# Kernel optimization log

Hardware: AMD Instinct MI355X
Metric: run time of the kernel (lower is better)

## Reference

```python
import jax, jax.numpy as jnp
import numpy as np

N_NODES = 50000
N_EDGES = 800000
N_GRAPHS = 8
D_IN, D_HID, D_OUT = 128, 128, 64


def setup_inputs() -> dict:
    key = jax.random.key(0)
    ks = jax.random.split(key, 8)
    x = jax.random.normal(ks[0], (N_NODES, D_IN), jnp.float32)
    src = jax.random.randint(ks[1], (N_EDGES,), 0, N_NODES, dtype=jnp.int32)
    dst = jax.random.randint(ks[2], (N_EDGES,), 0, N_NODES, dtype=jnp.int32)
    graph_id = jnp.sort(jax.random.randint(ks[3], (N_NODES,), 0, N_GRAPHS, dtype=jnp.int32))
    s1 = 1.0 / np.sqrt(D_IN)
    s2 = 1.0 / np.sqrt(D_HID)
    W1 = jax.random.normal(ks[4], (D_IN, D_HID), jnp.float32) * s1
    b1 = jnp.zeros((D_HID,), jnp.float32)
    W2 = jax.random.normal(ks[5], (D_HID, D_HID), jnp.float32) * s2
    b2 = jnp.zeros((D_HID,), jnp.float32)
    Wl = jax.random.normal(ks[6], (D_HID, D_OUT), jnp.float32) * s2
    bl = jnp.zeros((D_OUT,), jnp.float32)
    return dict(x=x, W1=W1, b1=b1, W2=W2, b2=b2, Wl=Wl, bl=bl,
                src=src, dst=dst, graph_id=graph_id)


def _graph_conv(x, W, b, src, dst):
    # DGL GraphConv, norm='both': h' = D_in^{-1/2} A (D_out^{-1/2} x W) + b
    n = x.shape[0]
    ones = jnp.ones((src.shape[0],), x.dtype)
    out_deg = jax.ops.segment_sum(ones, src, num_segments=n)
    in_deg = jax.ops.segment_sum(ones, dst, num_segments=n)
    norm_src = jax.lax.rsqrt(jnp.clip(out_deg, 1.0))  # [N]
    norm_dst = jax.lax.rsqrt(jnp.clip(in_deg, 1.0))   # [N]
    h = (x * norm_src[:, None]) @ W                    # [N, D]
    agg = jax.ops.segment_sum(h[src], dst, num_segments=n)  # gather-scatter SpMM
    return agg * norm_dst[:, None] + b


def reference(x, W1, b1, W2, b2, Wl, bl, src, dst, graph_id):
    h = jax.nn.relu(_graph_conv(x, W1, b1, src, dst))
    h = _graph_conv(h, W2, b2, src, dst)
    # dgl.mean_nodes over batched graph: per-graph mean of node features
    cnt = jax.ops.segment_sum(jnp.ones((x.shape[0],), x.dtype), graph_id,
                              num_segments=N_GRAPHS)
    pooled = jax.ops.segment_sum(h, graph_id, num_segments=N_GRAPHS)
    means = pooled / jnp.clip(cnt, 1.0)[:, None]       # [B, D_HID]
    return means @ Wl + bl                              # [B, D_OUT]
```

## Files before the change

kernel.cpp:

```cpp
#include <hip/hip_runtime.h>
#include <hip/hip_bf16.h>

#define N_NODES 50000
#define N_EDGES 800000
#define N_GRAPHS 8
#define MAXDEG 64
#define NRANGE 4
#define NCHUNK 64
#define RSZ (N_NODES / NRANGE)
#define CHE (N_EDGES / NCHUNK)

typedef __attribute__((ext_vector_type(8))) short short8;
typedef __attribute__((ext_vector_type(4))) float floatx4;
typedef __attribute__((ext_vector_type(2))) float floatx2;

static __device__ __forceinline__ ushort f2b(float f) {
    union { float f; unsigned u; } v; v.f = f;
    return (ushort)((v.u + 0x7FFF + ((v.u >> 16) & 1)) >> 16);
}
static __device__ __forceinline__ float b2f(unsigned u) {
    union { unsigned u; float f; } v; v.u = u << 16;
    return v.f;
}
static __device__ __forceinline__ unsigned char f2q(float f) {
    int p = __builtin_amdgcn_cvt_pk_fp8_f32(f, f, 0, false);
    return (unsigned char)(p & 0xff);
}

__global__ __launch_bounds__(1024) void prep_kernel(
    const int* __restrict__ src, const int* __restrict__ dst,
    const float* __restrict__ W1, const float* __restrict__ W2,
    const int* __restrict__ gid,
    ushort* __restrict__ counts_in, ushort* __restrict__ counts_out,
    ushort* __restrict__ Wt1, ushort* __restrict__ Wt2,
    int* __restrict__ start)
{
    int b = blockIdx.x, t = threadIdx.x;
    if (b < 256) {
        __shared__ unsigned h[RSZ];
        int c = b & (NCHUNK - 1), r = b >> 6;
        int lo = r * RSZ;
        for (int j = t; j < RSZ; j += 1024) h[j] = 0;
        __syncthreads();
        int ebeg = c * CHE, eend = ebeg + CHE;
        for (int i = ebeg + t; i < eend; i += 1024) {
            int s = src[i], d = dst[i];
            unsigned ds = (unsigned)(d - lo);
            if (ds < RSZ) atomicAdd(&h[ds >> 1], 1u << ((ds & 1) * 16));
            unsigned ss = (unsigned)(s - lo);
            if (ss < RSZ) atomicAdd(&h[(RSZ / 2) + (ss >> 1)], 1u << ((ss & 1) * 16));
        }
        __syncthreads();
        unsigned* ci = (unsigned*)(counts_in  + (size_t)c * N_NODES + lo);
        unsigned* co = (unsigned*)(counts_out + (size_t)c * N_NODES + lo);
        for (int j = t; j < RSZ / 2; j += 1024) {
            ci[j] = h[j];
            co[j] = h[(RSZ / 2) + j];
        }
    } else if (b < 272) {
        int i = (b - 256) * 1024 + t;
        int c = i >> 7, k = i & 127;
        Wt1[i] = f2b(W1[k * 128 + c]);
        Wt2[i] = f2b(W2[k * 128 + c]);
    } else {
        int i = (b - 272) * 1024 + t;
        if (i < N_NODES) {
            int g = gid[i];
            int gp = (i == 0) ? -1 : gid[i - 1];
            for (int k = gp + 1; k <= g; ++k) start[k] = i;
            if (i == N_NODES - 1)
                for (int k = g + 1; k <= N_GRAPHS; ++k) start[k] = N_NODES;
        }
    }
}

__global__ __launch_bounds__(256) void scan_kernel(
    const ushort* __restrict__ counts_in, const ushort* __restrict__ counts_out,
    ushort* __restrict__ base, int* __restrict__ in_deg,
    float* __restrict__ ns, float* __restrict__ nd)
{
    int v = blockIdx.x * 256 + threadIdx.x;
    if (v >= N_NODES) return;
    unsigned od = 0;
    #pragma unroll 8
    for (int c = 0; c < NCHUNK; ++c) od += counts_out[(size_t)c * N_NODES + v];
    unsigned run = 0;
    #pragma unroll 8
    for (int c = 0; c < NCHUNK; ++c) {
        base[(size_t)c * N_NODES + v] = (ushort)run;
        run += counts_in[(size_t)c * N_NODES + v];
    }
    in_deg[v] = (int)run;
    ns[v] = rsqrtf(fmaxf((float)od, 1.f));
    nd[v] = rsqrtf(fmaxf((float)run, 1.f));
}

__global__ __launch_bounds__(1024) void scatter_kernel(
    const int* __restrict__ src, const int* __restrict__ dst,
    const ushort* __restrict__ base, ushort* __restrict__ slot)
{
    __shared__ unsigned h[RSZ / 2];
    int t = threadIdx.x;
    int c = blockIdx.x & (NCHUNK - 1), r = blockIdx.x >> 6;
    int lo = r * RSZ;
    const unsigned* bp = (const unsigned*)(base + (size_t)c * N_NODES + lo);
    for (int j = t; j < RSZ / 2; j += 1024) h[j] = bp[j];
    __syncthreads();
    int ebeg = c * CHE, eend = ebeg + CHE;
    for (int i = ebeg + t; i < eend; i += 1024) {
        int d = dst[i];
        unsigned ds = (unsigned)(d - lo);
        if (ds < RSZ) {
            int sh = (ds & 1) * 16;
            unsigned old = atomicAdd(&h[ds >> 1], 1u << sh);
            unsigned pos = (old >> sh) & 0xffff;
            if (pos < MAXDEG) slot[(size_t)d * MAXDEG + pos] = (ushort)src[i];
        }
    }
}

template<int FP32_IN>
__global__ __launch_bounds__(256, 2) void mfma_gemm_kernel(
    const void* __restrict__ Xv, const float* __restrict__ scale,
    const ushort* __restrict__ Wt, unsigned char* __restrict__ Y, int n)
{
    int t = threadIdx.x;
    int wv = t >> 6, lane = t & 63;
    int m = lane & 15, q = lane >> 4;
    short8 B[8][4];
    #pragma unroll
    for (int cb = 0; cb < 8; ++cb)
        #pragma unroll
        for (int kb = 0; kb < 4; ++kb)
            B[cb][kb] = *(const short8*)&Wt[(size_t)(cb * 16 + m) * 128 + kb * 32 + q * 8];

    int ntile = n >> 4;
    int gw = blockIdx.x * 4 + wv;
    for (int tile = gw; tile < ntile; tile += 2048) {
        int row = tile * 16 + m;
        short8 a[4];
        if (FP32_IN) {
            const float* X = (const float*)Xv;
            float s = scale[row];
            #pragma unroll
            for (int kb = 0; kb < 4; ++kb) {
                const float* p = X + (size_t)row * 128 + kb * 32 + q * 8;
                float4 f0 = *(const float4*)p;
                float4 f1 = *(const float4*)(p + 4);
                short8 av;
                av[0] = (short)f2b(f0.x * s); av[1] = (short)f2b(f0.y * s);
                av[2] = (short)f2b(f0.z * s); av[3] = (short)f2b(f0.w * s);
                av[4] = (short)f2b(f1.x * s); av[5] = (short)f2b(f1.y * s);
                av[6] = (short)f2b(f1.z * s); av[7] = (short)f2b(f1.w * s);
                a[kb] = av;
            }
        } else {
            const ushort* X = (const ushort*)Xv;
            #pragma unroll
            for (int kb = 0; kb < 4; ++kb)
                a[kb] = *(const short8*)(X + (size_t)row * 128 + kb * 32 + q * 8);
        }
        floatx4 acc[8] = {};
        #pragma unroll
        for (int cb = 0; cb < 8; ++cb)
            #pragma unroll
            for (int kb = 0; kb < 4; ++kb)
                acc[cb] = __builtin_amdgcn_mfma_f32_16x16x32_bf16(a[kb], B[cb][kb], acc[cb], 0, 0, 0);
        int rowbase = tile * 16 + q * 4;
        #pragma unroll
        for (int cb = 0; cb < 8; ++cb)
            #pragma unroll
            for (int r = 0; r < 4; ++r)
                Y[(size_t)(rowbase + r) * 128 + cb * 16 + m] = f2q(acc[cb][r]);
    }
}

__global__ __launch_bounds__(256) void spmm_fp8_kernel(
    const unsigned char* __restrict__ H, const int* __restrict__ in_deg,
    const ushort* __restrict__ slot, const float* __restrict__ norm_dst,
    const float* __restrict__ norm_src, const float* __restrict__ bias,
    ushort* __restrict__ Y, int relu_scale)
{
    int wid = (blockIdx.x * blockDim.x + threadIdx.x) >> 6;
    if (wid >= N_NODES / 8) return;
    int lane = threadIdx.x & 63;
    int g = lane >> 3;
    int j = lane & 7;
    int node = wid * 8 + g;
    int cnt = min(in_deg[node], MAXDEG);
    float ndv = norm_dst[node];
    const ushort* lst = slot + (size_t)node * MAXDEG;

    int cm = cnt;
    cm = max(cm, __shfl_xor(cm, 8, 64));
    cm = max(cm, __shfl_xor(cm, 16, 64));
    cm = max(cm, __shfl_xor(cm, 32, 64));

    float acc[16] = {};
    for (int e0 = 0; e0 < cm; e0 += 8) {
        int sl = lst[e0 + j];
        #pragma unroll
        for (int k = 0; k < 8; ++k) {
            if (e0 + k < cnt) {
                int s = __shfl(sl, g * 8 + k, 64);
                uint4 v = *(const uint4*)&H[(size_t)s * 128 + j * 16];
                floatx2 p;
                p = __builtin_amdgcn_cvt_pk_f32_fp8((int)v.x, false); acc[0] += p.x;  acc[1] += p.y;
                p = __builtin_amdgcn_cvt_pk_f32_fp8((int)v.x, true);  acc[2] += p.x;  acc[3] += p.y;
                p = __builtin_amdgcn_cvt_pk_f32_fp8((int)v.y, false); acc[4] += p.x;  acc[5] += p.y;
                p = __builtin_amdgcn_cvt_pk_f32_fp8((int)v.y, true);  acc[6] += p.x;  acc[7] += p.y;
                p = __builtin_amdgcn_cvt_pk_f32_fp8((int)v.z, false); acc[8] += p.x;  acc[9] += p.y;
                p = __builtin_amdgcn_cvt_pk_f32_fp8((int)v.z, true);  acc[10] += p.x; acc[11] += p.y;
                p = __builtin_amdgcn_cvt_pk_f32_fp8((int)v.w, false); acc[12] += p.x; acc[13] += p.y;
                p = __builtin_amdgcn_cvt_pk_f32_fp8((int)v.w, true);  acc[14] += p.x; acc[15] += p.y;
            }
        }
    }

    int c16 = j * 16;
    float r[16];
    #pragma unroll
    for (int u = 0; u < 4; ++u) {
        float4 bv = *(const float4*)&bias[c16 + u * 4];
        r[u * 4 + 0] = acc[u * 4 + 0] * ndv + bv.x;
        r[u * 4 + 1] = acc[u * 4 + 1] * ndv + bv.y;
        r[u * 4 + 2] = acc[u * 4 + 2] * ndv + bv.z;
        r[u * 4 + 3] = acc[u * 4 + 3] * ndv + bv.w;
    }
    if (relu_scale) {
        float nsv = norm_src[node];
        #pragma unroll
        for (int u = 0; u < 16; ++u) r[u] = fmaxf(r[u], 0.f) * nsv;
    }
    uint4 o0, o1;
    o0.x = (unsigned)f2b(r[0])  | ((unsigned)f2b(r[1])  << 16);
    o0.y = (unsigned)f2b(r[2])  | ((unsigned)f2b(r[3])  << 16);
    o0.z = (unsigned)f2b(r[4])  | ((unsigned)f2b(r[5])  << 16);
    o0.w = (unsigned)f2b(r[6])  | ((unsigned)f2b(r[7])  << 16);
    o1.x = (unsigned)f2b(r[8])  | ((unsigned)f2b(r[9])  << 16);
    o1.y = (unsigned)f2b(r[10]) | ((unsigned)f2b(r[11]) << 16);
    o1.z = (unsigned)f2b(r[12]) | ((unsigned)f2b(r[13]) << 16);
    o1.w = (unsigned)f2b(r[14]) | ((unsigned)f2b(r[15]) << 16);
    uint4* yp = (uint4*)&Y[(size_t)node * 128 + c16];
    yp[0] = o0;
    yp[1] = o1;
}

__global__ __launch_bounds__(256) void pool_kernel(
    const ushort* __restrict__ H, const int* __restrict__ start,
    float* __restrict__ part)
{
    __shared__ float red[128];
    int t = threadIdx.x;
    int g = blockIdx.x >> 5, j = blockIdx.x & 31;
    int beg0 = start[g], len = start[g + 1] - beg0;
    int sbeg = beg0 + (int)(((long long)len * j) >> 5);
    int send = beg0 + (int)(((long long)len * (j + 1)) >> 5);
    int wv = t >> 6, lane = t & 63;
    int rg = lane >> 4;
    int c8 = (lane & 15) * 8;
    float acc[8] = {};
    for (int v = sbeg + wv * 4 + rg; v < send; v += 16) {
        uint4 u = *(const uint4*)&H[(size_t)v * 128 + c8];
        acc[0] += b2f(u.x & 0xffff); acc[1] += b2f(u.x >> 16);
        acc[2] += b2f(u.y & 0xffff); acc[3] += b2f(u.y >> 16);
        acc[4] += b2f(u.z & 0xffff); acc[5] += b2f(u.z >> 16);
        acc[6] += b2f(u.w & 0xffff); acc[7] += b2f(u.w >> 16);
    }
    #pragma unroll
    for (int k = 0; k < 8; ++k) {
        acc[k] += __shfl_xor(acc[k], 16, 64);
        acc[k] += __shfl_xor(acc[k], 32, 64);
    }
    if (t < 128) red[t] = 0.f;
    __syncthreads();
    if (lane < 16) {
        #pragma unroll
        for (int k = 0; k < 8; ++k) atomicAdd(&red[c8 + k], acc[k]);
    }
    __syncthreads();
    if (t < 128) part[(size_t)blockIdx.x * 128 + t] = red[t];
}

__global__ __launch_bounds__(512) void head_kernel(
    const float* __restrict__ part, const int* __restrict__ start,
    const float* __restrict__ Wl, const float* __restrict__ bl,
    float* __restrict__ out)
{
    __shared__ float means[N_GRAPHS * 128];
    int t = threadIdx.x;
    for (int i = t; i < N_GRAPHS * 128; i += 512) {
        int g = i >> 7, k = i & 127;
        float s = 0.f;
        #pragma unroll 8
        for (int j = 0; j < 32; ++j) s += part[(size_t)(g * 32 + j) * 128 + k];
        float cnt = (float)(start[g + 1] - start[g]);
        means[i] = s / fmaxf(cnt, 1.f);
    }
    __syncthreads();
    int g = t >> 6, c = t & 63;
    float acc = bl[c];
    #pragma unroll 8
    for (int k = 0; k < 128; ++k)
        acc = fmaf(means[g * 128 + k], Wl[k * 64 + c], acc);
    out[g * 64 + c] = acc;
}

extern "C" void kernel_launch(void* const* d_in, const int* in_sizes, int n_in,
                              void* d_out, int out_size, void* d_ws, size_t ws_size,
                              hipStream_t stream) {
    const float* x   = (const float*)d_in[0];
    const float* W1  = (const float*)d_in[1];
    const float* b1  = (const float*)d_in[2];
    const float* W2  = (const float*)d_in[3];
    const float* b2  = (const float*)d_in[4];
    const float* Wl  = (const float*)d_in[5];
    const float* bl  = (const float*)d_in[6];
    const int*   src = (const int*)d_in[7];
    const int*   dst = (const int*)d_in[8];
    const int*   gid = (const int*)d_in[9];

    const int n = N_NODES;

    char* ws = (char*)d_ws;
    size_t off = 0;
    auto alloc = [&](size_t bytes) { size_t o = off; off += (bytes + 255) & ~(size_t)255; return o; };
    unsigned char* hA = (unsigned char*)(ws + alloc((size_t)n * 128));
    ushort* hB        = (ushort*)(ws + alloc((size_t)n * 128 * 2));
    ushort* slot      = (ushort*)(ws + alloc((size_t)n * MAXDEG * 2));
    ushort* counts_in = (ushort*)(ws + alloc((size_t)NCHUNK * n * 2));
    ushort* counts_out= (ushort*)(ws + alloc((size_t)NCHUNK * n * 2));
    ushort* basev     = (ushort*)(ws + alloc((size_t)NCHUNK * n * 2));
    float* norm_src   = (float*) (ws + alloc((size_t)n * 4));
    float* norm_dst   = (float*) (ws + alloc((size_t)n * 4));
    int*   in_deg     = (int*)   (ws + alloc((size_t)n * 4));
    int*   startb     = (int*)   (ws + alloc((size_t)(N_GRAPHS + 1) * 4));
    ushort* Wt1       = (ushort*)(ws + alloc((size_t)128 * 128 * 2));
    ushort* Wt2       = (ushort*)(ws + alloc((size_t)128 * 128 * 2));
    float* part       = (float*) (ws + alloc((size_t)N_GRAPHS * 32 * 128 * 4));

    int spmm_blocks = (N_NODES / 8 + 3) / 4;

    prep_kernel<<<321, 1024, 0, stream>>>(src, dst, W1, W2, gid,
                                          counts_in, counts_out, Wt1, Wt2, startb);
    scan_kernel<<<(n + 255) / 256, 256, 0, stream>>>(counts_in, counts_out, basev,
                                                     in_deg, norm_src, norm_dst);
    scatter_kernel<<<NRANGE * NCHUNK, 1024, 0, stream>>>(src, dst, basev, slot);
    mfma_gemm_kernel<1><<<512, 256, 0, stream>>>(x, norm_src, Wt1, hA, n);
    spmm_fp8_kernel<<<spmm_blocks, 256, 0, stream>>>(hA, in_deg, slot, norm_dst,
                                                     norm_src, b1, hB, 1);
    mfma_gemm_kernel<0><<<512, 256, 0, stream>>>(hB, nullptr, Wt2, hA, n);
    spmm_fp8_kernel<<<spmm_blocks, 256, 0, stream>>>(hA, in_deg, slot, norm_dst,
                                                     nullptr, b2, hB, 0);
    pool_kernel<<<N_GRAPHS * 32, 256, 0, stream>>>(hB, startb, part);
    head_kernel<<<1, 512, 0, stream>>>(part, startb, Wl, bl, (float*)d_out);
}
```

Baseline: 199.7 us.

## Sort destination nodes by in-degree to balance SpMM wavefront work

Builds a degree histogram during the scan and adds a kernel that produces a permutation of nodes grouped by in-degree. Each SpMM wavefront then processes 8 nodes with similar degree, so the inner loop bound (the max degree among the 8) no longer wastes iterations on divergent lanes. The cost is one extra kernel launch, an indirect perm load, and scattered output rows, which lose the write locality of contiguous node order.

```diff
diff --git a/kernel.cpp b/kernel.cpp
--- a/kernel.cpp
+++ b/kernel.cpp
@@ -33,7 +33,7 @@
     const int* __restrict__ gid,
     ushort* __restrict__ counts_in, ushort* __restrict__ counts_out,
     ushort* __restrict__ Wt1, ushort* __restrict__ Wt2,
-    int* __restrict__ start)
+    int* __restrict__ start, unsigned* __restrict__ binz)
 {
     int b = blockIdx.x, t = threadIdx.x;
     if (b < 256) {
@@ -71,28 +71,61 @@
             if (i == N_NODES - 1)
                 for (int k = g + 1; k <= N_GRAPHS; ++k) start[k] = N_NODES;
         }
+        if (b == 320 && t >= 848 && t < 978) binz[t - 848] = 0;
     }
 }
 
 __global__ __launch_bounds__(256) void scan_kernel(
     const ushort* __restrict__ counts_in, const ushort* __restrict__ counts_out,
     ushort* __restrict__ base, int* __restrict__ in_deg,
-    float* __restrict__ ns, float* __restrict__ nd)
-{
-    int v = blockIdx.x * 256 + threadIdx.x;
-    if (v >= N_NODES) return;
-    unsigned od = 0;
-    #pragma unroll 8
-    for (int c = 0; c < NCHUNK; ++c) od += counts_out[(size_t)c * N_NODES + v];
-    unsigned run = 0;
-    #pragma unroll 8
-    for (int c = 0; c < NCHUNK; ++c) {
-        base[(size_t)c * N_NODES + v] = (ushort)run;
-        run += counts_in[(size_t)c * N_NODES + v];
-    }
-    in_deg[v] = (int)run;
-    ns[v] = rsqrtf(fmaxf((float)od, 1.f));
-    nd[v] = rsqrtf(fmaxf((float)run, 1.f));
+    float* __restrict__ ns, float* __restrict__ nd, unsigned* __restrict__ bins)
+{
+    __shared__ unsigned hist[MAXDEG + 1];
+    int t = threadIdx.x;
+    if (t < MAXDEG + 1) hist[t] = 0;
+    __syncthreads();
+    int v = blockIdx.x * 256 + t;
+    if (v < N_NODES) {
+        unsigned od = 0;
+        #pragma unroll 8
+        for (int c = 0; c < NCHUNK; ++c) od += counts_out[(size_t)c * N_NODES + v];
+        unsigned run = 0;
+        #pragma unroll 8
+        for (int c = 0; c < NCHUNK; ++c) {
+            base[(size_t)c * N_NODES + v] = (ushort)run;
+            run += counts_in[(size_t)c * N_NODES + v];
+        }
+        in_deg[v] = (int)run;
+        ns[v] = rsqrtf(fmaxf((float)od, 1.f));
+        nd[v] = rsqrtf(fmaxf((float)run, 1.f));
+        atomicAdd(&hist[min((int)run, MAXDEG)], 1u);
+    }
+    __syncthreads();
+    if (t < MAXDEG + 1 && hist[t]) atomicAdd(&bins[t], hist[t]);
+}
+
+__global__ __launch_bounds__(256) void perm_kernel(
+    const int* __restrict__ in_deg, const unsigned* __restrict__ bins,
+    unsigned* __restrict__ bincur, int* __restrict__ perm)
+{
+    __shared__ unsigned bh[MAXDEG + 1], bstart[MAXDEG + 1], sbin[MAXDEG + 1];
+    int t = threadIdx.x;
+    if (t < MAXDEG + 1) { bh[t] = 0; sbin[t] = bins[t]; }
+    __syncthreads();
+    int v = blockIdx.x * 256 + t;
+    int cb = 0; unsigned rank = 0;
+    if (v < N_NODES) {
+        cb = min(in_deg[v], MAXDEG);
+        rank = atomicAdd(&bh[cb], 1u);
+    }
+    __syncthreads();
+    if (t < MAXDEG + 1) {
+        unsigned b0 = 0;
+        for (int k = 0; k < t; ++k) b0 += sbin[k];
+        bstart[t] = b0 + atomicAdd(&bincur[t], bh[t]);
+    }
+    __syncthreads();
+    if (v < N_NODES) perm[bstart[cb] + rank] = v;
 }
 
 __global__ __launch_bounds__(1024) void scatter_kernel(
@@ -179,14 +212,14 @@
     const unsigned char* __restrict__ H, const int* __restrict__ in_deg,
     const ushort* __restrict__ slot, const float* __restrict__ norm_dst,
     const float* __restrict__ norm_src, const float* __restrict__ bias,
-    ushort* __restrict__ Y, int relu_scale)
+    const int* __restrict__ perm, ushort* __restrict__ Y, int relu_scale)
 {
     int wid = (blockIdx.x * blockDim.x + threadIdx.x) >> 6;
     if (wid >= N_NODES / 8) return;
     int lane = threadIdx.x & 63;
     int g = lane >> 3;
     int j = lane & 7;
-    int node = wid * 8 + g;
+    int node = perm[wid * 8 + g];
     int cnt = min(in_deg[node], MAXDEG);
     float ndv = norm_dst[node];
     const ushort* lst = slot + (size_t)node * MAXDEG;
@@ -338,20 +371,27 @@
     ushort* Wt1       = (ushort*)(ws + alloc((size_t)128 * 128 * 2));
     ushort* Wt2       = (ushort*)(ws + alloc((size_t)128 * 128 * 2));
     float* part       = (float*) (ws + alloc((size_t)N_GRAPHS * 32 * 128 * 4));
+    unsigned* binz    = (unsigned*)(ws + alloc((size_t)130 * 4));
+    int*   permv      = (int*)   (ws + alloc((size_t)n * 4));
+
+    unsigned* bins   = binz;
+    unsigned* bincur = binz + 65;
 
     int spmm_blocks = (N_NODES / 8 + 3) / 4;
+    int node_blocks = (n + 255) / 256;
 
     prep_kernel<<<321, 1024, 0, stream>>>(src, dst, W1, W2, gid,
-                                          counts_in, counts_out, Wt1, Wt2, startb);
-    scan_kernel<<<(n + 255) / 256, 256, 0, stream>>>(counts_in, counts_out, basev,
-                                                     in_deg, norm_src, norm_dst);
+                                          counts_in, counts_out, Wt1, Wt2, startb, binz);
+    scan_kernel<<<node_blocks, 256, 0, stream>>>(counts_in, counts_out, basev,
+                                                 in_deg, norm_src, norm_dst, bins);
+    perm_kernel<<<node_blocks, 256, 0, stream>>>(in_deg, bins, bincur, permv);
     scatter_kernel<<<NRANGE * NCHUNK, 1024, 0, stream>>>(src, dst, basev, slot);
     mfma_gemm_kernel<1><<<512, 256, 0, stream>>>(x, norm_src, Wt1, hA, n);
     spmm_fp8_kernel<<<spmm_blocks, 256, 0, stream>>>(hA, in_deg, slot, norm_dst,
-                                                     norm_src, b1, hB, 1);
+                                                     norm_src, b1, permv, hB, 1);
     mfma_gemm_kernel<0><<<512, 256, 0, stream>>>(hB, nullptr, Wt2, hA, n);
     spmm_fp8_kernel<<<spmm_blocks, 256, 0, stream>>>(hA, in_deg, slot, norm_dst,
-                                                     nullptr, b2, hB, 0);
+                                                     nullptr, b2, permv, hB, 0);
     pool_kernel<<<N_GRAPHS * 32, 256, 0, stream>>>(hB, startb, part);
     head_kernel<<<1, 512, 0, stream>>>(part, startb, Wl, bl, (float*)d_out);
 }
```

After: 208.0 us. 4.2% more time.

## Fuse mean-pool reduction into second SpMM and drop pool kernel

Applied to the files above, without the earlier changes.

The second SpMM now reduces its output rows per block in shared memory by graph id, using two slots per block because graph ids are sorted. It writes per-block partial sums instead of storing the bf16 hidden matrix, which removes the pool kernel and the write and reread of that matrix. The head kernel now accumulates those per-block partials per graph before the final linear layer. The two-slot scheme assumes each 32-node block spans at most two graphs, and the head kernel now performs a serial reduction over roughly 1.5k partials in a single block.

```diff
diff --git a/kernel.cpp b/kernel.cpp
--- a/kernel.cpp
+++ b/kernel.cpp
@@ -9,6 +9,7 @@
 #define NCHUNK 64
 #define RSZ (N_NODES / NRANGE)
 #define CHE (N_EDGES / NCHUNK)
+#define SPMM_BLOCKS ((N_NODES / 8 + 3) / 4)
 
 typedef __attribute__((ext_vector_type(8))) short short8;
 typedef __attribute__((ext_vector_type(4))) float floatx4;
@@ -175,135 +176,132 @@
     }
 }
 
+template<int POOL>
 __global__ __launch_bounds__(256) void spmm_fp8_kernel(
     const unsigned char* __restrict__ H, const int* __restrict__ in_deg,
     const ushort* __restrict__ slot, const float* __restrict__ norm_dst,
     const float* __restrict__ norm_src, const float* __restrict__ bias,
-    ushort* __restrict__ Y, int relu_scale)
-{
-    int wid = (blockIdx.x * blockDim.x + threadIdx.x) >> 6;
-    if (wid >= N_NODES / 8) return;
-    int lane = threadIdx.x & 63;
+    const int* __restrict__ gid, ushort* __restrict__ Y,
+    float* __restrict__ part2)
+{
+    __shared__ float red[256];
+    int tid = threadIdx.x;
+    int wid = (blockIdx.x * blockDim.x + tid) >> 6;
+    int lane = tid & 63;
+    bool act = wid < N_NODES / 8;
     int g = lane >> 3;
     int j = lane & 7;
-    int node = wid * 8 + g;
-    int cnt = min(in_deg[node], MAXDEG);
-    float ndv = norm_dst[node];
-    const ushort* lst = slot + (size_t)node * MAXDEG;
-
-    int cm = cnt;
-    cm = max(cm, __shfl_xor(cm, 8, 64));
-    cm = max(cm, __shfl_xor(cm, 16, 64));
-    cm = max(cm, __shfl_xor(cm, 32, 64));
-
-    float acc[16] = {};
-    for (int e0 = 0; e0 < cm; e0 += 8) {
-        int sl = lst[e0 + j];
-        #pragma unroll
-        for (int k = 0; k < 8; ++k) {
-            if (e0 + k < cnt) {
-                int s = __shfl(sl, g * 8 + k, 64);
-                uint4 v = *(const uint4*)&H[(size_t)s * 128 + j * 16];
-                floatx2 p;
-                p = __builtin_amdgcn_cvt_pk_f32_fp8((int)v.x, false); acc[0] += p.x;  acc[1] += p.y;
-                p = __builtin_amdgcn_cvt_pk_f32_fp8((int)v.x, true);  acc[2] += p.x;  acc[3] += p.y;
-                p = __builtin_amdgcn_cvt_pk_f32_fp8((int)v.y, false); acc[4] += p.x;  acc[5] += p.y;
-                p = __builtin_amdgcn_cvt_pk_f32_fp8((int)v.y, true);  acc[6] += p.x;  acc[7] += p.y;
-                p = __builtin_amdgcn_cvt_pk_f32_fp8((int)v.z, false); acc[8] += p.x;  acc[9] += p.y;
-                p = __builtin_amdgcn_cvt_pk_f32_fp8((int)v.z, true);  acc[10] += p.x; acc[11] += p.y;
-                p = __builtin_amdgcn_cvt_pk_f32_fp8((int)v.w, false); acc[12] += p.x; acc[13] += p.y;
-                p = __builtin_amdgcn_cvt_pk_f32_fp8((int)v.w, true);  acc[14] += p.x; acc[15] += p.y;
+    int node = act ? wid * 8 + g : 0;
+
+    if (POOL) red[tid] = 0.f;
+
+    float r[16];
+    if (act) {
+        int cnt = min(in_deg[node], MAXDEG);
+        float ndv = norm_dst[node];
+        const ushort* lst = slot + (size_t)node * MAXDEG;
+
+        int cm = cnt;
+        cm = max(cm, __shfl_xor(cm, 8, 64));
+        cm = max(cm, __shfl_xor(cm, 16, 64));
+        cm = max(cm, __shfl_xor(cm, 32, 64));
+
+        float acc[16] = {};
+        for (int e0 = 0; e0 < cm; e0 += 8) {
+            int sl = lst[e0 + j];
+            #pragma unroll
+            for (int k = 0; k < 8; ++k) {
+                if (e0 + k < cnt) {
+                    int s = __shfl(sl, g * 8 + k, 64);
+                    uint4 v = *(const uint4*)&H[(size_t)s * 128 + j * 16];
+                    floatx2 p;
+                    p = __builtin_amdgcn_cvt_pk_f32_fp8((int)v.x, false); acc[0] += p.x;  acc[1] += p.y;
+                    p = __builtin_amdgcn_cvt_pk_f32_fp8((int)v.x, true);  acc[2] += p.x;  acc[3] += p.y;
+                    p = __builtin_amdgcn_cvt_pk_f32_fp8((int)v.y, false); acc[4] += p.x;  acc[5] += p.y;
+                    p = __builtin_amdgcn_cvt_pk_f32_fp8((int)v.y, true);  acc[6] += p.x;  acc[7] += p.y;
+                    p = __builtin_amdgcn_cvt_pk_f32_fp8((int)v.z, false); acc[8] += p.x;  acc[9] += p.y;
+                    p = __builtin_amdgcn_cvt_pk_f32_fp8((int)v.z, true);  acc[10] += p.x; acc[11] += p.y;
+                    p = __builtin_amdgcn_cvt_pk_f32_fp8((int)v.w, false); acc[12] += p.x; acc[13] += p.y;
+                    p = __builtin_amdgcn_cvt_pk_f32_fp8((int)v.w, true);  acc[14] += p.x; acc[15] += p.y;
+                }
             }
         }
-    }
-
-    int c16 = j * 16;
-    float r[16];
-    #pragma unroll
-    for (int u = 0; u < 4; ++u) {
-        float4 bv = *(const float4*)&bias[c16 + u * 4];
-        r[u * 4 + 0] = acc[u * 4 + 0] * ndv + bv.x;
-        r[u * 4 + 1] = acc[u * 4 + 1] * ndv + bv.y;
-        r[u * 4 + 2] = acc[u * 4 + 2] * ndv + bv.z;
-        r[u * 4 + 3] = acc[u * 4 + 3] * ndv + bv.w;
-    }
-    if (relu_scale) {
+
+        int c16 = j * 16;
+        #pragma unroll
+        for (int u = 0; u < 4; ++u) {
+            float4 bv = *(const float4*)&bias[c16 + u * 4];
+            r[u * 4 + 0] = acc[u * 4 + 0] * ndv + bv.x;
+            r[u * 4 + 1] = acc[u * 4 + 1] * ndv + bv.y;
+            r[u * 4 + 2] = acc[u * 4 + 2] * ndv + bv.z;
+            r[u * 4 + 3] = acc[u * 4 + 3] * ndv + bv.w;
+        }
+    }
+
+    if (POOL) {
+        __syncthreads();
+        if (act) {
+            int lg = gid[node] - gid[blockIdx.x * 32];
+            lg = lg < 1 ? 0 : 1;
+            int base = lg * 128 + j * 16;
+            #pragma unroll
+            for (int u = 0; u < 16; ++u) atomicAdd(&red[base + u], r[u]);
+        }
+        __syncthreads();
+        part2[(size_t)blockIdx.x * 256 + tid] = red[tid];
+    } else if (act) {
         float nsv = norm_src[node];
         #pragma unroll
         for (int u = 0; u < 16; ++u) r[u] = fmaxf(r[u], 0.f) * nsv;
-    }
-    uint4 o0, o1;
-    o0.x = (unsigned)f2b(r[0])  | ((unsigned)f2b(r[1])  << 16);
-    o0.y = (unsigned)f2b(r[2])  | ((unsigned)f2b(r[3])  << 16);
-    o0.z = (unsigned)f2b(r[4])  | ((unsigned)f2b(r[5])  << 16);
-    o0.w = (unsigned)f2b(r[6])  | ((unsigned)f2b(r[7])  << 16);
-    o1.x = (unsigned)f2b(r[8])  | ((unsigned)f2b(r[9])  << 16);
-    o1.y = (unsigned)f2b(r[10]) | ((unsigned)f2b(r[11]) << 16);
-    o1.z = (unsigned)f2b(r[12]) | ((unsigned)f2b(r[13]) << 16);
-    o1.w = (unsigned)f2b(r[14]) | ((unsigned)f2b(r[15]) << 16);
-    uint4* yp = (uint4*)&Y[(size_t)node * 128 + c16];
-    yp[0] = o0;
-    yp[1] = o1;
-}
-
-__global__ __launch_bounds__(256) void pool_kernel(
-    const ushort* __restrict__ H, const int* __restrict__ start,
-    float* __restrict__ part)
-{
-    __shared__ float red[128];
-    int t = threadIdx.x;
-    int g = blockIdx.x >> 5, j = blockIdx.x & 31;
-    int beg0 = start[g], len = start[g + 1] - beg0;
-    int sbeg = beg0 + (int)(((long long)len * j) >> 5);
-    int send = beg0 + (int)(((long long)len * (j + 1)) >> 5);
-    int wv = t >> 6, lane = t & 63;
-    int rg = lane >> 4;
-    int c8 = (lane & 15) * 8;
-    float acc[8] = {};
-    for (int v = sbeg + wv * 4 + rg; v < send; v += 16) {
-        uint4 u = *(const uint4*)&H[(size_t)v * 128 + c8];
-        acc[0] += b2f(u.x & 0xffff); acc[1] += b2f(u.x >> 16);
-        acc[2] += b2f(u.y & 0xffff); acc[3] += b2f(u.y >> 16);
-        acc[4] += b2f(u.z & 0xffff); acc[5] += b2f(u.z >> 16);
-        acc[6] += b2f(u.w & 0xffff); acc[7] += b2f(u.w >> 16);
-    }
-    #pragma unroll
-    for (int k = 0; k < 8; ++k) {
-        acc[k] += __shfl_xor(acc[k], 16, 64);
-        acc[k] += __shfl_xor(acc[k], 32, 64);
-    }
-    if (t < 128) red[t] = 0.f;
-    __syncthreads();
-    if (lane < 16) {
-        #pragma unroll
-        for (int k = 0; k < 8; ++k) atomicAdd(&red[c8 + k], acc[k]);
-    }
-    __syncthreads();
-    if (t < 128) part[(size_t)blockIdx.x * 128 + t] = red[t];
-}
-
-__global__ __launch_bounds__(512) void head_kernel(
-    const float* __restrict__ part, const int* __restrict__ start,
-    const float* __restrict__ Wl, const float* __restrict__ bl,
-    float* __restrict__ out)
-{
+        uint4 o0, o1;
+        o0.x = (unsigned)f2b(r[0])  | ((unsigned)f2b(r[1])  << 16);
+        o0.y = (unsigned)f2b(r[2])  | ((unsigned)f2b(r[3])  << 16);
+        o0.z = (unsigned)f2b(r[4])  | ((unsigned)f2b(r[5])  << 16);
+        o0.w = (unsigned)f2b(r[6])  | ((unsigned)f2b(r[7])  << 16);
+        o1.x = (unsigned)f2b(r[8])  | ((unsigned)f2b(r[9])  << 16);
+        o1.y = (unsigned)f2b(r[10]) | ((unsigned)f2b(r[11]) << 16);
+        o1.z = (unsigned)f2b(r[12]) | ((unsigned)f2b(r[13]) << 16);
+        o1.w = (unsigned)f2b(r[14]) | ((unsigned)f2b(r[15]) << 16);
+        uint4* yp = (uint4*)&Y[(size_t)node * 128 + j * 16];
+        yp[0] = o0;
+        yp[1] = o1;
+    }
+}
+
+__global__ __launch_bounds__(1024) void head_kernel(
+    const float* __restrict__ part2, const int* __restrict__ start,
+    const int* __restrict__ gid, const float* __restrict__ Wl,
+    const float* __restrict__ bl, float* __restrict__ out)
+{
+    __shared__ float ac[8][N_GRAPHS][128];
     __shared__ float means[N_GRAPHS * 128];
     int t = threadIdx.x;
-    for (int i = t; i < N_GRAPHS * 128; i += 512) {
-        int g = i >> 7, k = i & 127;
-        float s = 0.f;
+    for (int i = t; i < 8 * N_GRAPHS * 128; i += 1024) ((float*)ac)[i] = 0.f;
+    __syncthreads();
+    int s = t >> 7, c = t & 127;
+    for (int b = s; b < SPMM_BLOCKS; b += 8) {
+        int gb = gid[b * 32];
+        ac[s][gb][c] += part2[(size_t)b * 256 + c];
+        if (gb + 1 < N_GRAPHS) ac[s][gb + 1][c] += part2[(size_t)b * 256 + 128 + c];
+    }
+    __syncthreads();
+    if (t < N_GRAPHS * 128) {
+        int g = t >> 7, k = t & 127;
+        float ssum = 0.f;
+        #pragma unroll
+        for (int q = 0; q < 8; ++q) ssum += ac[q][g][k];
+        float cnt = (float)(start[g + 1] - start[g]);
+        means[t] = ssum / fmaxf(cnt, 1.f);
+    }
+    __syncthreads();
+    if (t < N_GRAPHS * 64) {
+        int g = t >> 6, c2 = t & 63;
+        float acc = bl[c2];
         #pragma unroll 8
-        for (int j = 0; j < 32; ++j) s += part[(size_t)(g * 32 + j) * 128 + k];
-        float cnt = (float)(start[g + 1] - start[g]);
-        means[i] = s / fmaxf(cnt, 1.f);
-    }
-    __syncthreads();
-    int g = t >> 6, c = t & 63;
-    float acc = bl[c];
-    #pragma unroll 8
-    for (int k = 0; k < 128; ++k)
-        acc = fmaf(means[g * 128 + k], Wl[k * 64 + c], acc);
-    out[g * 64 + c] = acc;
+        for (int k = 0; k < 128; ++k)
+            acc = fmaf(means[g * 128 + k], Wl[k * 64 + c2], acc);
+        out[g * 64 + c2] = acc;
+    }
 }
 
 extern "C" void kernel_launch(void* const* d_in, const int* in_sizes, int n_in,
@@ -337,9 +335,7 @@
     int*   startb     = (int*)   (ws + alloc((size_t)(N_GRAPHS + 1) * 4));
     ushort* Wt1       = (ushort*)(ws + alloc((size_t)128 * 128 * 2));
     ushort* Wt2       = (ushort*)(ws + alloc((size_t)128 * 128 * 2));
-    float* part       = (float*) (ws + alloc((size_t)N_GRAPHS * 32 * 128 * 4));
-
-    int spmm_blocks = (N_NODES / 8 + 3) / 4;
+    float* part2      = (float*) (ws + alloc((size_t)SPMM_BLOCKS * 256 * 4));
 
     prep_kernel<<<321, 1024, 0, stream>>>(src, dst, W1, W2, gid,
                                           counts_in, counts_out, Wt1, Wt2, startb);
@@ -347,11 +343,10 @@
                                                      in_deg, norm_src, norm_dst);
     scatter_kernel<<<NRANGE * NCHUNK, 1024, 0, stream>>>(src, dst, basev, slot);
     mfma_gemm_kernel<1><<<512, 256, 0, stream>>>(x, norm_src, Wt1, hA, n);
-    spmm_fp8_kernel<<<spmm_blocks, 256, 0, stream>>>(hA, in_deg, slot, norm_dst,
-                                                     norm_src, b1, hB, 1);
+    spmm_fp8_kernel<0><<<SPMM_BLOCKS, 256, 0, stream>>>(hA, in_deg, slot, norm_dst,
+                                                        norm_src, b1, gid, hB, nullptr);
     mfma_gemm_kernel<0><<<512, 256, 0, stream>>>(hB, nullptr, Wt2, hA, n);
-    spmm_fp8_kernel<<<spmm_blocks, 256, 0, stream>>>(hA, in_deg, slot, norm_dst,
-                                                     nullptr, b2, hB, 0);
-    pool_kernel<<<N_GRAPHS * 32, 256, 0, stream>>>(hB, startb, part);
-    head_kernel<<<1, 512, 0, stream>>>(part, startb, Wl, bl, (float*)d_out);
-}
+    spmm_fp8_kernel<1><<<SPMM_BLOCKS, 256, 0, stream>>>(hA, in_deg, slot, norm_dst,
+                                                        nullptr, b2, gid, nullptr, part2);
+    head_kernel<<<1, 1024, 0, stream>>>(part2, startb, gid, Wl, bl, (float*)d_out);
+}
```

Result: slower. 331.6 us (+66.1%).

## Split fp8 feature matrix into column planes for cache-resident SpMM gathers

Applied to the files above, without the earlier changes.

The GEMM now writes its fp8 output as two 64-column planes instead of 128-wide rows. Each SpMM layer runs as two launches, one per plane, with 4 lanes per node and 16 nodes per wave. The aim is to keep each plane's gather footprint small enough to stay in cache, cutting random-access misses. In exchange, the adjacency lists, degrees and norms are read twice, kernel launches double, and each gathered row segment is half as large.

```diff
diff --git a/kernel.cpp b/kernel.cpp
--- a/kernel.cpp
+++ b/kernel.cpp
@@ -9,6 +9,7 @@
 #define NCHUNK 64
 #define RSZ (N_NODES / NRANGE)
 #define CHE (N_EDGES / NCHUNK)
+#define PLANE_BYTES ((size_t)N_NODES * 64)
 
 typedef __attribute__((ext_vector_type(8))) short short8;
 typedef __attribute__((ext_vector_type(4))) float floatx4;
@@ -168,42 +169,47 @@
                 acc[cb] = __builtin_amdgcn_mfma_f32_16x16x32_bf16(a[kb], B[cb][kb], acc[cb], 0, 0, 0);
         int rowbase = tile * 16 + q * 4;
         #pragma unroll
-        for (int cb = 0; cb < 8; ++cb)
+        for (int cb = 0; cb < 8; ++cb) {
+            size_t pb = (cb < 4) ? 0 : PLANE_BYTES;
+            int pc = (cb & 3) * 16 + m;
             #pragma unroll
             for (int r = 0; r < 4; ++r)
-                Y[(size_t)(rowbase + r) * 128 + cb * 16 + m] = f2q(acc[cb][r]);
-    }
-}
-
-__global__ __launch_bounds__(256) void spmm_fp8_kernel(
-    const unsigned char* __restrict__ H, const int* __restrict__ in_deg,
+                Y[pb + (size_t)(rowbase + r) * 64 + pc] = f2q(acc[cb][r]);
+        }
+    }
+}
+
+__global__ __launch_bounds__(256) void spmm_plane_kernel(
+    const unsigned char* __restrict__ Hp, const int* __restrict__ in_deg,
     const ushort* __restrict__ slot, const float* __restrict__ norm_dst,
     const float* __restrict__ norm_src, const float* __restrict__ bias,
-    ushort* __restrict__ Y, int relu_scale)
+    ushort* __restrict__ Y, int colbase, int relu_scale)
 {
     int wid = (blockIdx.x * blockDim.x + threadIdx.x) >> 6;
-    if (wid >= N_NODES / 8) return;
+    if (wid >= N_NODES / 16) return;
     int lane = threadIdx.x & 63;
-    int g = lane >> 3;
-    int j = lane & 7;
-    int node = wid * 8 + g;
+    int g = lane >> 2;
+    int j = lane & 3;
+    int node = wid * 16 + g;
     int cnt = min(in_deg[node], MAXDEG);
     float ndv = norm_dst[node];
     const ushort* lst = slot + (size_t)node * MAXDEG;
 
     int cm = cnt;
+    cm = max(cm, __shfl_xor(cm, 4, 64));
     cm = max(cm, __shfl_xor(cm, 8, 64));
     cm = max(cm, __shfl_xor(cm, 16, 64));
     cm = max(cm, __shfl_xor(cm, 32, 64));
 
     float acc[16] = {};
     for (int e0 = 0; e0 < cm; e0 += 8) {
-        int sl = lst[e0 + j];
-        #pragma unroll
-        for (int k = 0; k < 8; ++k) {
+        int sl0 = lst[e0 + j];
+        int sl1 = lst[e0 + 4 + j];
+        #pragma unroll
+        for (int k = 0; k < 4; ++k) {
             if (e0 + k < cnt) {
-                int s = __shfl(sl, g * 8 + k, 64);
-                uint4 v = *(const uint4*)&H[(size_t)s * 128 + j * 16];
+                int s = __shfl(sl0, g * 4 + k, 64);
+                uint4 v = *(const uint4*)&Hp[(size_t)s * 64 + j * 16];
                 floatx2 p;
                 p = __builtin_amdgcn_cvt_pk_f32_fp8((int)v.x, false); acc[0] += p.x;  acc[1] += p.y;
                 p = __builtin_amdgcn_cvt_pk_f32_fp8((int)v.x, true);  acc[2] += p.x;  acc[3] += p.y;
@@ -215,13 +221,29 @@
                 p = __builtin_amdgcn_cvt_pk_f32_fp8((int)v.w, true);  acc[14] += p.x; acc[15] += p.y;
             }
         }
-    }
-
-    int c16 = j * 16;
+        #pragma unroll
+        for (int k = 0; k < 4; ++k) {
+            if (e0 + 4 + k < cnt) {
+                int s = __shfl(sl1, g * 4 + k, 64);
+                uint4 v = *(const uint4*)&Hp[(size_t)s * 64 + j * 16];
+                floatx2 p;
+                p = __builtin_amdgcn_cvt_pk_f32_fp8((int)v.x, false); acc[0] += p.x;  acc[1] += p.y;
+                p = __builtin_amdgcn_cvt_pk_f32_fp8((int)v.x, true);  acc[2] += p.x;  acc[3] += p.y;
+                p = __builtin_amdgcn_cvt_pk_f32_fp8((int)v.y, false); acc[4] += p.x;  acc[5] += p.y;
+                p = __builtin_amdgcn_cvt_pk_f32_fp8((int)v.y, true);  acc[6] += p.x;  acc[7] += p.y;
+                p = __builtin_amdgcn_cvt_pk_f32_fp8((int)v.z, false); acc[8] += p.x;  acc[9] += p.y;
+                p = __builtin_amdgcn_cvt_pk_f32_fp8((int)v.z, true);  acc[10] += p.x; acc[11] += p.y;
+                p = __builtin_amdgcn_cvt_pk_f32_fp8((int)v.w, false); acc[12] += p.x; acc[13] += p.y;
+                p = __builtin_amdgcn_cvt_pk_f32_fp8((int)v.w, true);  acc[14] += p.x; acc[15] += p.y;
+            }
+        }
+    }
+
+    int col = colbase + j * 16;
     float r[16];
     #pragma unroll
     for (int u = 0; u < 4; ++u) {
-        float4 bv = *(const float4*)&bias[c16 + u * 4];
+        float4 bv = *(const float4*)&bias[col + u * 4];
         r[u * 4 + 0] = acc[u * 4 + 0] * ndv + bv.x;
         r[u * 4 + 1] = acc[u * 4 + 1] * ndv + bv.y;
         r[u * 4 + 2] = acc[u * 4 + 2] * ndv + bv.z;
@@ -241,7 +263,7 @@
     o1.y = (unsigned)f2b(r[10]) | ((unsigned)f2b(r[11]) << 16);
     o1.z = (unsigned)f2b(r[12]) | ((unsigned)f2b(r[13]) << 16);
     o1.w = (unsigned)f2b(r[14]) | ((unsigned)f2b(r[15]) << 16);
-    uint4* yp = (uint4*)&Y[(size_t)node * 128 + c16];
+    uint4* yp = (uint4*)&Y[(size_t)node * 128 + col];
     yp[0] = o0;
     yp[1] = o1;
 }
@@ -325,7 +347,7 @@
     char* ws = (char*)d_ws;
     size_t off = 0;
     auto alloc = [&](size_t bytes) { size_t o = off; off += (bytes + 255) & ~(size_t)255; return o; };
-    unsigned char* hA = (unsigned char*)(ws + alloc((size_t)n * 128));
+    unsigned char* hA = (unsigned char*)(ws + alloc(2 * PLANE_BYTES));
     ushort* hB        = (ushort*)(ws + alloc((size_t)n * 128 * 2));
     ushort* slot      = (ushort*)(ws + alloc((size_t)n * MAXDEG * 2));
     ushort* counts_in = (ushort*)(ws + alloc((size_t)NCHUNK * n * 2));
@@ -339,7 +361,10 @@
     ushort* Wt2       = (ushort*)(ws + alloc((size_t)128 * 128 * 2));
     float* part       = (float*) (ws + alloc((size_t)N_GRAPHS * 32 * 128 * 4));
 
-    int spmm_blocks = (N_NODES / 8 + 3) / 4;
+    const unsigned char* plane0 = hA;
+    const unsigned char* plane1 = hA + PLANE_BYTES;
+
+    int spmm_blocks = (N_NODES / 16 * 64 + 255) / 256;
 
     prep_kernel<<<321, 1024, 0, stream>>>(src, dst, W1, W2, gid,
                                           counts_in, counts_out, Wt1, Wt2, startb);
@@ -347,11 +372,15 @@
                                                      in_deg, norm_src, norm_dst);
     scatter_kernel<<<NRANGE * NCHUNK, 1024, 0, stream>>>(src, dst, basev, slot);
     mfma_gemm_kernel<1><<<512, 256, 0, stream>>>(x, norm_src, Wt1, hA, n);
-    spmm_fp8_kernel<<<spmm_blocks, 256, 0, stream>>>(hA, in_deg, slot, norm_dst,
-                                                     norm_src, b1, hB, 1);
+    spmm_plane_kernel<<<spmm_blocks, 256, 0, stream>>>(plane0, in_deg, slot, norm_dst,
+                                                       norm_src, b1, hB, 0, 1);
+    spmm_plane_kernel<<<spmm_blocks, 256, 0, stream>>>(plane1, in_deg, slot, norm_dst,
+                                                       norm_src, b1, hB, 64, 1);
     mfma_gemm_kernel<0><<<512, 256, 0, stream>>>(hB, nullptr, Wt2, hA, n);
-    spmm_fp8_kernel<<<spmm_blocks, 256, 0, stream>>>(hA, in_deg, slot, norm_dst,
-                                                     nullptr, b2, hB, 0);
+    spmm_plane_kernel<<<spmm_blocks, 256, 0, stream>>>(plane0, in_deg, slot, norm_dst,
+                                                       nullptr, b2, hB, 0, 0);
+    spmm_plane_kernel<<<spmm_blocks, 256, 0, stream>>>(plane1, in_deg, slot, norm_dst,
+                                                       nullptr, b2, hB, 64, 0);
     pool_kernel<<<N_GRAPHS * 32, 256, 0, stream>>>(hB, startb, part);
     head_kernel<<<1, 512, 0, stream>>>(part, startb, Wl, bl, (float*)d_out);
 }
```

New measurement: 220.7 us. +10.5%, slower.
